# Performance work log

Measured on AMD Instinct MI355X. Metric: run time of the kernel, lower is better.

The kernel has to match this reference:

```python
import jax, jax.numpy as jnp
import numpy as np

N = 100000   # total nodes in batch
E = 1200000  # total edges
D = 64       # dim_features (== hidden_dim)
H = 64       # hidden_dim
T = 32       # dim_targets
L = 3        # num_layers
G = 500      # number of graphs in batch


def setup_inputs() -> dict:
    key = jax.random.key(0)
    ks = jax.random.split(key, 16)
    s = 0.1
    inp = {
        "x": jax.random.normal(ks[0], (N, D), jnp.float32),
        "src": jax.random.randint(ks[1], (E,), 0, N, jnp.int32),
        "dst": jax.random.randint(ks[2], (E,), 0, N, jnp.int32),
        "graph_ids": jnp.sort(jax.random.randint(ks[3], (N,), 0, G, jnp.int32)),
        # GINConv learnable eps (init 0)
        "eps": jnp.zeros((L,), jnp.float32),
        # per-layer conv apply MLP: Linear(D->H), ReLU, Linear(H->H)
        "conv_w1": jax.random.normal(ks[4], (L, D, H), jnp.float32) * s,
        "conv_b1": jnp.zeros((L, H), jnp.float32),
        "conv_w2": jax.random.normal(ks[5], (L, H, H), jnp.float32) * s,
        "conv_b2": jnp.zeros((L, H), jnp.float32),
        # GraphNorm params
        "gn_weight": jnp.ones((L, H), jnp.float32),
        "gn_bias": jnp.zeros((L, H), jnp.float32),
        "gn_scale": jnp.ones((L, H), jnp.float32),
        # per-layer projection MLP: Linear(H->H), ReLU, Linear(H->T)
        "proj_w1": jax.random.normal(ks[6], (L, H, H), jnp.float32) * s,
        "proj_b1": jnp.zeros((L, H), jnp.float32),
        "proj_w2": jax.random.normal(ks[7], (L, H, T), jnp.float32) * s,
        "proj_b2": jnp.zeros((L, T), jnp.float32),
    }
    return inp


def reference(x, src, dst, graph_ids, eps, conv_w1, conv_b1, conv_w2, conv_b2,
              gn_weight, gn_bias, gn_scale, proj_w1, proj_b1, proj_w2, proj_b2):
    gid = graph_ids
    counts = jax.ops.segment_sum(jnp.ones((N,), x.dtype), gid, num_segments=G)
    safe = jnp.maximum(counts, 1.0)[:, None]  # [G,1] nodes per graph

    feat = x
    outs = []
    for l in range(L):
        # GINConv: (1+eps)*h_i + sum over incoming neighbors
        agg = jax.ops.segment_sum(feat[src], dst, num_segments=N)
        h = (1.0 + eps[l]) * feat + agg
        h = jnp.maximum(h @ conv_w1[l] + conv_b1[l], 0.0) @ conv_w2[l] + conv_b2[l]
        # GraphNorm: per-graph mean/std
        mean = jax.ops.segment_sum(h, gid, num_segments=G) / safe
        sub = h - mean[gid] * gn_scale[l]
        var = jax.ops.segment_sum(sub * sub, gid, num_segments=G) / safe
        std = jnp.sqrt(var + 1e-8)
        h = gn_weight[l] * sub / std[gid] + gn_bias[l]
        feat = jnp.maximum(h, 0.0)
        # projection MLP + per-graph mean pooling
        z = jnp.maximum(feat @ proj_w1[l] + proj_b1[l], 0.0) @ proj_w2[l] + proj_b2[l]
        outs.append(jax.ops.segment_sum(z, gid, num_segments=G) / safe)
    return jnp.concatenate(outs, axis=-1)  # [G, L*T]
```

## Files before the change

kernel.cpp:

```cpp
#include <hip/hip_runtime.h>
#include <math.h>

#define N_NODES 100000
#define N_EDGES 1200000
#define DIM 64
#define TDIM 32
#define NLAYERS 3
#define NGRAPH 500
#define NP (N_NODES + 1)

#define BUCKW 512
#define NBUCK ((N_NODES + BUCKW - 1) / BUCKW)
#define ECHUNK ((N_EDGES + 255) / 256)

typedef unsigned short bfu;
typedef __attribute__((ext_vector_type(8))) short short8;
typedef __attribute__((ext_vector_type(4))) float v4f;

__device__ __forceinline__ float bf2f(bfu u) {
    union { unsigned int i; float f; } v; v.i = ((unsigned int)u) << 16; return v.f;
}
__device__ __forceinline__ float bflo(unsigned int d) {
    union { unsigned int i; float f; } v; v.i = d << 16; return v.f;
}
__device__ __forceinline__ float bfhi(unsigned int d) {
    union { unsigned int i; float f; } v; v.i = d & 0xFFFF0000u; return v.f;
}
__device__ __forceinline__ bfu f2bf(float f) {
    union { float f; unsigned int i; } v; v.f = f;
    unsigned int r = v.i + 0x7FFFu + ((v.i >> 16) & 1u);
    return (bfu)(r >> 16);
}


__global__ __launch_bounds__(512) void k_graph_start(const int* __restrict__ gid,
                                                     int* __restrict__ gstart,
                                                     float* __restrict__ inv_safe) {
    int t = threadIdx.x;
    if (t <= NGRAPH) {
        int lo = 0, hi = N_NODES;
        while (lo < hi) {
            int mid = (lo + hi) >> 1;
            if (gid[mid] < t) lo = mid + 1; else hi = mid;
        }
        gstart[t] = lo;
    }
    __syncthreads();
    if (t < NGRAPH) {
        int c = gstart[t + 1] - gstart[t];
        inv_safe[t] = 1.0f / (float)(c > 1 ? c : 1);
    }
}

__global__ __launch_bounds__(256) void k_wprep(const float* __restrict__ w1, const float* __restrict__ w2,
                                               const float* __restrict__ q1, const float* __restrict__ q2,
                                               bfu* __restrict__ w1t, bfu* __restrict__ w2t,
                                               bfu* __restrict__ q1t, bfu* __restrict__ q2t) {
    int i = blockIdx.x * 256 + threadIdx.x;
    if (i < NLAYERS * 4096) {
        int l = i >> 12, k = (i >> 6) & 63, n = i & 63;
        int o = (l << 12) | (n << 6) | k;
        w1t[o] = f2bf(w1[i]);
        w2t[o] = f2bf(w2[i]);
        q1t[o] = f2bf(q1[i]);
    }
    if (i < NLAYERS * 2048) {
        int l = i >> 11, rem = i & 2047, k = rem >> 5, n = rem & 31;
        q2t[l * 2048 + n * 64 + k] = f2bf(q2[i]);
    }
}


__global__ __launch_bounds__(256) void k_bhist(const int* __restrict__ dst, int* __restrict__ bcnt) {
    __shared__ int h[NBUCK];
    int t = threadIdx.x;
    for (int i = t; i < NBUCK; i += 256) h[i] = 0;
    __syncthreads();
    int e0 = blockIdx.x * ECHUNK;
    int e1 = e0 + ECHUNK; if (e1 > N_EDGES) e1 = N_EDGES;
    for (int e = e0 + t; e < e1; e += 256) atomicAdd(&h[dst[e] >> 9], 1);
    __syncthreads();
    for (int i = t; i < NBUCK; i += 256) if (h[i]) atomicAdd(&bcnt[i], h[i]);
}

__global__ __launch_bounds__(256) void k_bscan(const int* __restrict__ bcnt,
                                               int* __restrict__ bbase, int* __restrict__ bcursor) {
    __shared__ int s[256];
    int t = threadIdx.x;
    s[t] = (t < NBUCK) ? bcnt[t] : 0;
    __syncthreads();
    for (int off = 1; off < 256; off <<= 1) {
        int v = (t >= off) ? s[t - off] : 0;
        __syncthreads();
        s[t] += v;
        __syncthreads();
    }
    int ex = t ? s[t - 1] : 0;
    if (t < NBUCK) { bbase[t] = ex; bcursor[t] = ex; }
    if (t == 0) bbase[NBUCK] = N_EDGES;
}

__global__ __launch_bounds__(256) void k_bscatter(const int* __restrict__ src, const int* __restrict__ dst,
                                                  int* __restrict__ bcursor, int2* __restrict__ ebuf) {
    __shared__ int cnt[NBUCK];
    __shared__ int base[NBUCK];
    int t = threadIdx.x;
    for (int i = t; i < NBUCK; i += 256) cnt[i] = 0;
    __syncthreads();
    int e0 = blockIdx.x * ECHUNK;
    int e1 = e0 + ECHUNK; if (e1 > N_EDGES) e1 = N_EDGES;
    for (int e = e0 + t; e < e1; e += 256) atomicAdd(&cnt[dst[e] >> 9], 1);
    __syncthreads();
    for (int i = t; i < NBUCK; i += 256) base[i] = cnt[i] ? atomicAdd(&bcursor[i], cnt[i]) : 0;
    __syncthreads();
    for (int i = t; i < NBUCK; i += 256) cnt[i] = 0;
    __syncthreads();
    for (int e = e0 + t; e < e1; e += 256) {
        int d = dst[e];
        int b = d >> 9;
        int r = atomicAdd(&cnt[b], 1);
        ebuf[base[b] + r] = make_int2(src[e], d);
    }
}

__global__ __launch_bounds__(256) void k_bcsr(const int2* __restrict__ ebuf, const int* __restrict__ bbase,
                                              int* __restrict__ offs, int* __restrict__ csr) {
    __shared__ int ldeg[BUCKW];
    __shared__ int lscan[BUCKW];
    __shared__ int lcur[BUCKW];
    int t = threadIdx.x;
    int b = blockIdx.x;
    int nbase = b << 9;
    int ebeg = bbase[b], eend = bbase[b + 1];
    ldeg[t] = 0; ldeg[t + 256] = 0;
    __syncthreads();
    for (int e = ebeg + t; e < eend; e += 256) atomicAdd(&ldeg[ebuf[e].y - nbase], 1);
    __syncthreads();
    lscan[t] = ldeg[t]; lscan[t + 256] = ldeg[t + 256];
    __syncthreads();
    for (int off = 1; off < BUCKW; off <<= 1) {
        int i0 = t, i1 = t + 256;
        int v0 = (i0 >= off) ? lscan[i0 - off] : 0;
        int v1 = (i1 >= off) ? lscan[i1 - off] : 0;
        __syncthreads();
        lscan[i0] += v0; lscan[i1] += v1;
        __syncthreads();
    }
    int ex0 = lscan[t] - ldeg[t];
    int ex1 = lscan[t + 256] - ldeg[t + 256];
    lcur[t] = ex0; lcur[t + 256] = ex1;
    int n0 = nbase + t, n1 = nbase + t + 256;
    if (n0 < N_NODES) offs[n0] = ebeg + ex0;
    if (n1 < N_NODES) offs[n1] = ebeg + ex1;
    if (b == 0 && t == 0) offs[N_NODES] = N_EDGES;
    __syncthreads();
    for (int e = ebeg + t; e < eend; e += 256) {
        int2 p = ebuf[e];
        int slot = atomicAdd(&lcur[p.y - nbase], 1);
        csr[ebeg + slot] = p.x;
    }
}

__global__ __launch_bounds__(256) void k_x2bf(const float* __restrict__ x, bfu* __restrict__ xb) {
    int i = blockIdx.x * 256 + threadIdx.x;
    int base = i * 4;
    float4 v = *(const float4*)&x[base];
    ushort4 o;
    o.x = f2bf(v.x); o.y = f2bf(v.y); o.z = f2bf(v.z); o.w = f2bf(v.w);
    *(ushort4*)&xb[base] = o;
}

__device__ __forceinline__ void accum8(float* acc, uint4 d) {
    acc[0] += bflo(d.x); acc[1] += bfhi(d.x);
    acc[2] += bflo(d.y); acc[3] += bfhi(d.y);
    acc[4] += bflo(d.z); acc[5] += bfhi(d.z);
    acc[6] += bflo(d.w); acc[7] += bfhi(d.w);
}

__global__ __launch_bounds__(256) void k_agg(const bfu* __restrict__ feat, const int* __restrict__ offs,
                                             const int* __restrict__ csr, const float* __restrict__ eps,
                                             int l, bfu* __restrict__ hin) {
    int w = threadIdx.x >> 6;
    int lane = threadIdx.x & 63;
    int node = blockIdx.x * 4 + w;
    if (node >= N_NODES) return;
    int eidx = lane >> 3;
    int chunk = lane & 7;
    int coff = chunk * 8;
    int e0 = offs[node], e1 = offs[node + 1];
    int eL = e1 - 1;
    float acc[8] = {0.f, 0.f, 0.f, 0.f, 0.f, 0.f, 0.f, 0.f};

    for (int e = e0; e < e1; e += 16) {
        int ea = e + eidx;
        int ca = (ea < eL) ? ea : eL;
        int sa = csr[ca];
        uint4 da = *(const uint4*)&feat[sa * DIM + coff];
        bool two = (e + 8) < e1;
        if (two) {
            int ebi = e + 8 + eidx;
            int cb = (ebi < eL) ? ebi : eL;
            int sb = csr[cb];
            uint4 db = *(const uint4*)&feat[sb * DIM + coff];
            if (ea >= e1) da = make_uint4(0u, 0u, 0u, 0u);
            if (ebi >= e1) db = make_uint4(0u, 0u, 0u, 0u);
            accum8(acc, da);
            accum8(acc, db);
        } else {
            if (ea >= e1) da = make_uint4(0u, 0u, 0u, 0u);
            accum8(acc, da);
        }
    }

#pragma unroll
    for (int j = 0; j < 8; j++) {
        float v = acc[j];
        v += __shfl_xor(v, 8, 64);
        v += __shfl_xor(v, 16, 64);
        v += __shfl_xor(v, 32, 64);
        acc[j] = v;
    }

    float ep = 1.0f + eps[l];
    uint4 s = *(const uint4*)&feat[node * DIM + coff];
    float r0 = ep * bflo(s.x) + acc[0], r1 = ep * bfhi(s.x) + acc[1];
    float r2 = ep * bflo(s.y) + acc[2], r3 = ep * bfhi(s.y) + acc[3];
    float r4 = ep * bflo(s.z) + acc[4], r5 = ep * bfhi(s.z) + acc[5];
    float r6 = ep * bflo(s.w) + acc[6], r7 = ep * bfhi(s.w) + acc[7];
    if (eidx == 0) {
        uint4 o;
        o.x = ((unsigned int)f2bf(r1) << 16) | f2bf(r0);
        o.y = ((unsigned int)f2bf(r3) << 16) | f2bf(r2);
        o.z = ((unsigned int)f2bf(r5) << 16) | f2bf(r4);
        o.w = ((unsigned int)f2bf(r7) << 16) | f2bf(r6);
        *(uint4*)&hin[node * DIM + coff] = o;
    }
}

__global__ __launch_bounds__(256) void k_mlp(const bfu* __restrict__ hin,
                                             const bfu* __restrict__ w1t, const float* __restrict__ b1,
                                             const bfu* __restrict__ w2t, const float* __restrict__ b2,
                                             bfu* __restrict__ hout) {
    __shared__ bfu ldsT[4][16 * 80];
    int t = threadIdx.x;
    int w = t >> 6, lane = t & 63, m = lane & 15, q = lane >> 4;
    int row0 = blockIdx.x * 64;
    int row = row0 + w * 16 + m;
    bool valid = row < N_NODES;

    short8 a0 = {0, 0, 0, 0, 0, 0, 0, 0}, a1 = a0;
    if (valid) {
        a0 = *(const short8*)&hin[row * 64 + q * 8];
        a1 = *(const short8*)&hin[row * 64 + 32 + q * 8];
    }
    short8 bf1[4][2], bf2[4][2];
#pragma unroll
    for (int ct = 0; ct < 4; ct++)
#pragma unroll
        for (int kk = 0; kk < 2; kk++) {
            bf1[ct][kk] = *(const short8*)&w1t[(ct * 16 + m) * 64 + kk * 32 + q * 8];
            bf2[ct][kk] = *(const short8*)&w2t[(ct * 16 + m) * 64 + kk * 32 + q * 8];
        }

    bfu* tl = ldsT[w];
#pragma unroll
    for (int ct = 0; ct < 4; ct++) {
        float bv = b1[ct * 16 + m];
        v4f acc = {bv, bv, bv, bv};
        acc = __builtin_amdgcn_mfma_f32_16x16x32_bf16(a0, bf1[ct][0], acc, 0, 0, 0);
        acc = __builtin_amdgcn_mfma_f32_16x16x32_bf16(a1, bf1[ct][1], acc, 0, 0, 0);
#pragma unroll
        for (int r = 0; r < 4; r++)
            tl[(q * 4 + r) * 80 + ct * 16 + m] = f2bf(fmaxf(acc[r], 0.f));
    }
    short8 a20 = *(short8*)&tl[m * 80 + q * 8];
    short8 a21 = *(short8*)&tl[m * 80 + 32 + q * 8];
#pragma unroll
    for (int ct = 0; ct < 4; ct++) {
        float bv = b2[ct * 16 + m];
        v4f acc = {bv, bv, bv, bv};
        acc = __builtin_amdgcn_mfma_f32_16x16x32_bf16(a20, bf2[ct][0], acc, 0, 0, 0);
        acc = __builtin_amdgcn_mfma_f32_16x16x32_bf16(a21, bf2[ct][1], acc, 0, 0, 0);
#pragma unroll
        for (int r = 0; r < 4; r++)
            tl[(q * 4 + r) * 80 + ct * 16 + m] = f2bf(acc[r]);
    }
#pragma unroll
    for (int i = 0; i < 2; i++) {
        int idx = i * 64 + lane;
        int r = idx >> 3, ch = (idx & 7) * 8;
        int grow = row0 + w * 16 + r;
        uint4 v = *(uint4*)&tl[r * 80 + ch];
        if (grow < N_NODES) *(uint4*)&hout[grow * 64 + ch] = v;
    }
}

__global__ __launch_bounds__(256) void k_stats(const bfu* __restrict__ h,
                                               const int* __restrict__ gstart,
                                               const float* __restrict__ inv_safe,
                                               const float* __restrict__ gnw, const float* __restrict__ gns,
                                               const float* __restrict__ pb2,
                                               float* __restrict__ gms, float* __restrict__ gcoef,
                                               float* __restrict__ out, int l) {
    __shared__ float sRS[4][64];
    __shared__ float sRQ[4][64];
    int t = threadIdx.x;
    int g = blockIdx.x;
    int s = gstart[g], e = gstart[g + 1];
    int nn = e - s;
    float inv = inv_safe[g];
    int lane = t & 63, q = t >> 6;
    float sum = 0.f, sumsq = 0.f;
    for (int i = s + q; i < e; i += 4) {
        float v = bf2f(h[i * 64 + lane]);
        sum += v;
        sumsq += v * v;
    }
    sRS[q][lane] = sum;
    sRQ[q][lane] = sumsq;
    __syncthreads();
    if (t < 64) {
        float S = sRS[0][t] + sRS[1][t] + sRS[2][t] + sRS[3][t];
        float Q = sRQ[0][t] + sRQ[1][t] + sRQ[2][t] + sRQ[3][t];
        float m = S * inv;
        float ms = m * gns[t];
        float var = (Q - 2.f * ms * S + (float)nn * ms * ms) * inv;
        gms[g * 64 + t] = ms;
        gcoef[g * 64 + t] = gnw[t] * rsqrtf(var + 1e-8f);
    }
    if (t < TDIM) {
        out[g * (NLAYERS * TDIM) + l * TDIM + t] = (nn > 0) ? pb2[t] : 0.f;
    }
}

__global__ __launch_bounds__(256) void k_apply_proj(const bfu* __restrict__ h,
                                                    const int* __restrict__ gid,
                                                    const float* __restrict__ gms,
                                                    const float* __restrict__ gcoef,
                                                    const float* __restrict__ gnb,
                                                    const float* __restrict__ inv_safe,
                                                    const bfu* __restrict__ p1t, const float* __restrict__ pb1,
                                                    const bfu* __restrict__ p2t,
                                                    bfu* __restrict__ feat, float* __restrict__ out, int l) {
    __shared__ bfu ldsT[4][16 * 80];
    __shared__ float sZ[64 * 33];
    __shared__ int sGid[64];
    int t = threadIdx.x;
    int w = t >> 6, lane = t & 63, m = lane & 15, q = lane >> 4;
    int row0 = blockIdx.x * 64;
    int row = row0 + w * 16 + m;
    bool valid = row < N_NODES;
    if (t < 64) sGid[t] = (row0 + t < N_NODES) ? gid[row0 + t] : -1;

    union Pack { short8 v; bfu u[8]; uint4 qv; };
    Pack a0, a1;
    a0.qv = make_uint4(0u, 0u, 0u, 0u);
    a1.qv = make_uint4(0u, 0u, 0u, 0u);
    if (valid) {
        int g = gid[row];
#pragma unroll
        for (int kk = 0; kk < 2; kk++) {
            int ch = kk * 32 + q * 8;
            uint4 hv = *(const uint4*)&h[row * 64 + ch];
            float4 msa = *(const float4*)&gms[g * 64 + ch];
            float4 msb = *(const float4*)&gms[g * 64 + ch + 4];
            float4 cfa = *(const float4*)&gcoef[g * 64 + ch];
            float4 cfb = *(const float4*)&gcoef[g * 64 + ch + 4];
            float4 gba = *(const float4*)&gnb[ch];
            float4 gbb = *(const float4*)&gnb[ch + 4];
            Pack& a = kk ? a1 : a0;
            a.u[0] = f2bf(fmaxf(cfa.x * (bflo(hv.x) - msa.x) + gba.x, 0.f));
            a.u[1] = f2bf(fmaxf(cfa.y * (bfhi(hv.x) - msa.y) + gba.y, 0.f));
            a.u[2] = f2bf(fmaxf(cfa.z * (bflo(hv.y) - msa.z) + gba.z, 0.f));
            a.u[3] = f2bf(fmaxf(cfa.w * (bfhi(hv.y) - msa.w) + gba.w, 0.f));
            a.u[4] = f2bf(fmaxf(cfb.x * (bflo(hv.z) - msb.x) + gbb.x, 0.f));
            a.u[5] = f2bf(fmaxf(cfb.y * (bfhi(hv.z) - msb.y) + gbb.y, 0.f));
            a.u[6] = f2bf(fmaxf(cfb.z * (bflo(hv.w) - msb.z) + gbb.z, 0.f));
            a.u[7] = f2bf(fmaxf(cfb.w * (bfhi(hv.w) - msb.w) + gbb.w, 0.f));
            *(uint4*)&feat[row * 64 + ch] = a.qv;
        }
    }

    short8 bf1[4][2], bf2[2][2];
#pragma unroll
    for (int ct = 0; ct < 4; ct++)
#pragma unroll
        for (int kk = 0; kk < 2; kk++)
            bf1[ct][kk] = *(const short8*)&p1t[(ct * 16 + m) * 64 + kk * 32 + q * 8];
#pragma unroll
    for (int ct = 0; ct < 2; ct++)
#pragma unroll
        for (int kk = 0; kk < 2; kk++)
            bf2[ct][kk] = *(const short8*)&p2t[(ct * 16 + m) * 64 + kk * 32 + q * 8];

    bfu* tl = ldsT[w];
#pragma unroll
    for (int ct = 0; ct < 4; ct++) {
        float bv = pb1[ct * 16 + m];
        v4f acc = {bv, bv, bv, bv};
        acc = __builtin_amdgcn_mfma_f32_16x16x32_bf16(a0.v, bf1[ct][0], acc, 0, 0, 0);
        acc = __builtin_amdgcn_mfma_f32_16x16x32_bf16(a1.v, bf1[ct][1], acc, 0, 0, 0);
#pragma unroll
        for (int r = 0; r < 4; r++)
            tl[(q * 4 + r) * 80 + ct * 16 + m] = f2bf(fmaxf(acc[r], 0.f));
    }
    short8 a20 = *(short8*)&tl[m * 80 + q * 8];
    short8 a21 = *(short8*)&tl[m * 80 + 32 + q * 8];
#pragma unroll
    for (int ct = 0; ct < 2; ct++) {
        v4f acc = {0.f, 0.f, 0.f, 0.f};
        acc = __builtin_amdgcn_mfma_f32_16x16x32_bf16(a20, bf2[ct][0], acc, 0, 0, 0);
        acc = __builtin_amdgcn_mfma_f32_16x16x32_bf16(a21, bf2[ct][1], acc, 0, 0, 0);
#pragma unroll
        for (int r = 0; r < 4; r++)
            sZ[(w * 16 + q * 4 + r) * 33 + ct * 16 + m] = acc[r];
    }
    __syncthreads();

    if (t < 32) {
        int cur = sGid[0];
        float a = 0.f;
        for (int r = 0; r < 64; r++) {
            int g2 = sGid[r];
            if (g2 != cur) {
                if (cur >= 0) atomicAdd(&out[cur * (NLAYERS * TDIM) + l * TDIM + t], a * inv_safe[cur]);
                cur = g2;
                a = 0.f;
            }
            if (g2 >= 0) a += sZ[r * 33 + t];
        }
        if (cur >= 0) atomicAdd(&out[cur * (NLAYERS * TDIM) + l * TDIM + t], a * inv_safe[cur]);
    }
}


extern "C" void kernel_launch(void* const* d_in, const int* in_sizes, int n_in,
                              void* d_out, int out_size, void* d_ws, size_t ws_size,
                              hipStream_t stream) {
    const float* x        = (const float*)d_in[0];
    const int*   src      = (const int*)d_in[1];
    const int*   dst      = (const int*)d_in[2];
    const int*   gid      = (const int*)d_in[3];
    const float* eps      = (const float*)d_in[4];
    const float* conv_w1  = (const float*)d_in[5];
    const float* conv_b1  = (const float*)d_in[6];
    const float* conv_w2  = (const float*)d_in[7];
    const float* conv_b2  = (const float*)d_in[8];
    const float* gn_w     = (const float*)d_in[9];
    const float* gn_b     = (const float*)d_in[10];
    const float* gn_s     = (const float*)d_in[11];
    const float* proj_w1  = (const float*)d_in[12];
    const float* proj_b1  = (const float*)d_in[13];
    const float* proj_w2  = (const float*)d_in[14];
    const float* proj_b2  = (const float*)d_in[15];
    float* out = (float*)d_out;

    char* ws = (char*)d_ws;
    size_t off = 0;
    auto alloc = [&](size_t bytes) { char* p = ws + off; off += (bytes + 255) & ~(size_t)255; return p; };
    int*   offs     = (int*)alloc(NP * sizeof(int));
    int*   gstart   = (int*)alloc((NGRAPH + 1) * sizeof(int));
    float* inv_safe = (float*)alloc(NGRAPH * sizeof(float));
    int*   bcnt     = (int*)alloc(NBUCK * sizeof(int));
    int*   bbase    = (int*)alloc((NBUCK + 1) * sizeof(int));
    int*   bcursor  = (int*)alloc(NBUCK * sizeof(int));
    int*   csr      = (int*)alloc(N_EDGES * sizeof(int));
    bfu*   featbf   = (bfu*)alloc((size_t)N_NODES * DIM * sizeof(bfu));
    bfu*   hinbf    = (bfu*)alloc((size_t)N_NODES * DIM * sizeof(bfu));
    bfu*   hbufbf   = (bfu*)alloc((size_t)N_NODES * DIM * sizeof(bfu));
    float* gms      = (float*)alloc((size_t)NGRAPH * 64 * sizeof(float));
    float* gcoef    = (float*)alloc((size_t)NGRAPH * 64 * sizeof(float));
    bfu*   w1t      = (bfu*)alloc((size_t)NLAYERS * 4096 * sizeof(bfu));
    bfu*   w2t      = (bfu*)alloc((size_t)NLAYERS * 4096 * sizeof(bfu));
    bfu*   p1t      = (bfu*)alloc((size_t)NLAYERS * 4096 * sizeof(bfu));
    bfu*   p2t      = (bfu*)alloc((size_t)NLAYERS * 2048 * sizeof(bfu));
    int2*  ebuf     = (int2*)alloc((size_t)N_EDGES * sizeof(int2));

    k_graph_start<<<1, 512, 0, stream>>>(gid, gstart, inv_safe);
    hipMemsetAsync(bcnt, 0, NBUCK * sizeof(int), stream);
    k_bhist<<<256, 256, 0, stream>>>(dst, bcnt);
    k_bscan<<<1, 256, 0, stream>>>(bcnt, bbase, bcursor);
    k_bscatter<<<256, 256, 0, stream>>>(src, dst, bcursor, ebuf);
    k_bcsr<<<NBUCK, 256, 0, stream>>>(ebuf, bbase, offs, csr);
    k_x2bf<<<(N_NODES * DIM / 4) / 256, 256, 0, stream>>>(x, featbf);
    k_wprep<<<48, 256, 0, stream>>>(conv_w1, conv_w2, proj_w1, proj_w2, w1t, w2t, p1t, p2t);

    int aggbl = (N_NODES + 3) / 4;
    int mlpbl = (N_NODES + 63) / 64;
    for (int l = 0; l < NLAYERS; l++) {
        k_agg<<<aggbl, 256, 0, stream>>>(featbf, offs, csr, eps, l, hinbf);
        k_mlp<<<mlpbl, 256, 0, stream>>>(hinbf, w1t + l * 4096, conv_b1 + l * 64,
                                         w2t + l * 4096, conv_b2 + l * 64, hbufbf);
        k_stats<<<NGRAPH, 256, 0, stream>>>(hbufbf, gstart, inv_safe,
                                            gn_w + l * 64, gn_s + l * 64, proj_b2 + l * 32,
                                            gms, gcoef, out, l);
        k_apply_proj<<<mlpbl, 256, 0, stream>>>(hbufbf, gid, gms, gcoef, gn_b + l * 64,
                                                inv_safe, p1t + l * 4096, proj_b1 + l * 64,
                                                p2t + l * 2048, featbf, out, l);
    }
}
```

Before: 455.3 us.

## Fuse aggregation, conv MLP and GraphNorm stats; merge setup kernels

Neighbour aggregation is merged into the conv MLP kernel. Each wave aggregates its 16 nodes into LDS and then runs the MFMA MLP, so the hin round-trip through global memory goes away. Per-graph sum and sum-of-squares are now accumulated with atomics in the MLP epilogue instead of a separate pass that re-reads h, and a small finalize kernel computes the coefficients and zeros the accumulators. The setup kernels (x to bf16, graph starts, weight prep) are combined into one launch. The cost is less parallelism during aggregation, since each wave now handles 16 nodes one after another, plus float atomic contention.

Result: slower. 474.8 us (+4.3%).

```diff
diff --git a/kernel.cpp b/kernel.cpp
--- a/kernel.cpp
+++ b/kernel.cpp
@@ -12,6 +12,7 @@
 #define BUCKW 512
 #define NBUCK ((N_NODES + BUCKW - 1) / BUCKW)
 #define ECHUNK ((N_EDGES + 255) / 256)
+#define MLPBL ((N_NODES + 63) / 64)
 
 typedef unsigned short bfu;
 typedef __attribute__((ext_vector_type(8))) short short8;
@@ -32,41 +33,45 @@
     return (bfu)(r >> 16);
 }
 
-
-__global__ __launch_bounds__(512) void k_graph_start(const int* __restrict__ gid,
-                                                     int* __restrict__ gstart,
-                                                     float* __restrict__ inv_safe) {
-    int t = threadIdx.x;
-    if (t <= NGRAPH) {
-        int lo = 0, hi = N_NODES;
-        while (lo < hi) {
-            int mid = (lo + hi) >> 1;
-            if (gid[mid] < t) lo = mid + 1; else hi = mid;
-        }
-        gstart[t] = lo;
-    }
-    __syncthreads();
-    if (t < NGRAPH) {
-        int c = gstart[t + 1] - gstart[t];
-        inv_safe[t] = 1.0f / (float)(c > 1 ? c : 1);
-    }
-}
-
-__global__ __launch_bounds__(256) void k_wprep(const float* __restrict__ w1, const float* __restrict__ w2,
+__global__ __launch_bounds__(256) void k_setup(const float* __restrict__ x, bfu* __restrict__ xb,
+                                               const int* __restrict__ gid, int* __restrict__ gstart,
+                                               float* __restrict__ inv_safe,
+                                               const float* __restrict__ w1, const float* __restrict__ w2,
                                                const float* __restrict__ q1, const float* __restrict__ q2,
                                                bfu* __restrict__ w1t, bfu* __restrict__ w2t,
                                                bfu* __restrict__ q1t, bfu* __restrict__ q2t) {
-    int i = blockIdx.x * 256 + threadIdx.x;
-    if (i < NLAYERS * 4096) {
+    int b = blockIdx.x, t = threadIdx.x;
+    if (b < 6250) {
+        int base = (b * 256 + t) * 4;
+        float4 v = *(const float4*)&x[base];
+        ushort4 o;
+        o.x = f2bf(v.x); o.y = f2bf(v.y); o.z = f2bf(v.z); o.w = f2bf(v.w);
+        *(ushort4*)&xb[base] = o;
+    } else if (b == 6250) {
+        for (int tt = t; tt <= NGRAPH; tt += 256) {
+            int lo = 0, hi = N_NODES;
+            while (lo < hi) {
+                int mid = (lo + hi) >> 1;
+                if (gid[mid] < tt) lo = mid + 1; else hi = mid;
+            }
+            gstart[tt] = lo;
+        }
+        __syncthreads();
+        for (int tt = t; tt < NGRAPH; tt += 256) {
+            int c = gstart[tt + 1] - gstart[tt];
+            inv_safe[tt] = 1.0f / (float)(c > 1 ? c : 1);
+        }
+    } else {
+        int i = (b - 6251) * 256 + t;
         int l = i >> 12, k = (i >> 6) & 63, n = i & 63;
         int o = (l << 12) | (n << 6) | k;
         w1t[o] = f2bf(w1[i]);
         w2t[o] = f2bf(w2[i]);
         q1t[o] = f2bf(q1[i]);
-    }
-    if (i < NLAYERS * 2048) {
-        int l = i >> 11, rem = i & 2047, k = rem >> 5, n = rem & 31;
-        q2t[l * 2048 + n * 64 + k] = f2bf(q2[i]);
+        if (i < NLAYERS * 2048) {
+            int l2 = i >> 11, rem = i & 2047, k2 = rem >> 5, n2 = rem & 31;
+            q2t[l2 * 2048 + n2 * 64 + k2] = f2bf(q2[i]);
+        }
     }
 }
 
@@ -161,15 +166,6 @@
     }
 }
 
-__global__ __launch_bounds__(256) void k_x2bf(const float* __restrict__ x, bfu* __restrict__ xb) {
-    int i = blockIdx.x * 256 + threadIdx.x;
-    int base = i * 4;
-    float4 v = *(const float4*)&x[base];
-    ushort4 o;
-    o.x = f2bf(v.x); o.y = f2bf(v.y); o.z = f2bf(v.z); o.w = f2bf(v.w);
-    *(ushort4*)&xb[base] = o;
-}
-
 __device__ __forceinline__ void accum8(float* acc, uint4 d) {
     acc[0] += bflo(d.x); acc[1] += bfhi(d.x);
     acc[2] += bflo(d.y); acc[3] += bfhi(d.y);
@@ -177,82 +173,74 @@
     acc[6] += bflo(d.w); acc[7] += bfhi(d.w);
 }
 
-__global__ __launch_bounds__(256) void k_agg(const bfu* __restrict__ feat, const int* __restrict__ offs,
-                                             const int* __restrict__ csr, const float* __restrict__ eps,
-                                             int l, bfu* __restrict__ hin) {
-    int w = threadIdx.x >> 6;
-    int lane = threadIdx.x & 63;
-    int node = blockIdx.x * 4 + w;
-    if (node >= N_NODES) return;
-    int eidx = lane >> 3;
-    int chunk = lane & 7;
-    int coff = chunk * 8;
-    int e0 = offs[node], e1 = offs[node + 1];
-    int eL = e1 - 1;
-    float acc[8] = {0.f, 0.f, 0.f, 0.f, 0.f, 0.f, 0.f, 0.f};
-
-    for (int e = e0; e < e1; e += 16) {
-        int ea = e + eidx;
-        int ca = (ea < eL) ? ea : eL;
-        int sa = csr[ca];
-        uint4 da = *(const uint4*)&feat[sa * DIM + coff];
-        bool two = (e + 8) < e1;
-        if (two) {
-            int ebi = e + 8 + eidx;
-            int cb = (ebi < eL) ? ebi : eL;
-            int sb = csr[cb];
-            uint4 db = *(const uint4*)&feat[sb * DIM + coff];
-            if (ea >= e1) da = make_uint4(0u, 0u, 0u, 0u);
-            if (ebi >= e1) db = make_uint4(0u, 0u, 0u, 0u);
-            accum8(acc, da);
-            accum8(acc, db);
-        } else {
-            if (ea >= e1) da = make_uint4(0u, 0u, 0u, 0u);
-            accum8(acc, da);
-        }
-    }
-
-#pragma unroll
-    for (int j = 0; j < 8; j++) {
-        float v = acc[j];
-        v += __shfl_xor(v, 8, 64);
-        v += __shfl_xor(v, 16, 64);
-        v += __shfl_xor(v, 32, 64);
-        acc[j] = v;
-    }
-
+__global__ __launch_bounds__(256, 4) void k_agg_mlp(const bfu* __restrict__ feat,
+                                                    const int* __restrict__ offs, const int* __restrict__ csr,
+                                                    const float* __restrict__ eps, int l,
+                                                    const bfu* __restrict__ w1t, const float* __restrict__ b1,
+                                                    const bfu* __restrict__ w2t, const float* __restrict__ b2,
+                                                    const int* __restrict__ gid,
+                                                    bfu* __restrict__ hout,
+                                                    float* __restrict__ gsum, float* __restrict__ gsq) {
+    __shared__ bfu ldsT[4][16 * 80];
+    __shared__ int sG[4][16];
+    int t = threadIdx.x;
+    int w = t >> 6, lane = t & 63, m = lane & 15, q = lane >> 4;
+    int nbase = blockIdx.x * 64 + w * 16;
+    bfu* my = ldsT[w];
+    int eidx = lane >> 3, chunk = lane & 7, coff = chunk * 8;
     float ep = 1.0f + eps[l];
-    uint4 s = *(const uint4*)&feat[node * DIM + coff];
-    float r0 = ep * bflo(s.x) + acc[0], r1 = ep * bfhi(s.x) + acc[1];
-    float r2 = ep * bflo(s.y) + acc[2], r3 = ep * bfhi(s.y) + acc[3];
-    float r4 = ep * bflo(s.z) + acc[4], r5 = ep * bfhi(s.z) + acc[5];
-    float r6 = ep * bflo(s.w) + acc[6], r7 = ep * bfhi(s.w) + acc[7];
-    if (eidx == 0) {
-        uint4 o;
-        o.x = ((unsigned int)f2bf(r1) << 16) | f2bf(r0);
-        o.y = ((unsigned int)f2bf(r3) << 16) | f2bf(r2);
-        o.z = ((unsigned int)f2bf(r5) << 16) | f2bf(r4);
-        o.w = ((unsigned int)f2bf(r7) << 16) | f2bf(r6);
-        *(uint4*)&hin[node * DIM + coff] = o;
-    }
-}
-
-__global__ __launch_bounds__(256) void k_mlp(const bfu* __restrict__ hin,
-                                             const bfu* __restrict__ w1t, const float* __restrict__ b1,
-                                             const bfu* __restrict__ w2t, const float* __restrict__ b2,
-                                             bfu* __restrict__ hout) {
-    __shared__ bfu ldsT[4][16 * 80];
-    int t = threadIdx.x;
-    int w = t >> 6, lane = t & 63, m = lane & 15, q = lane >> 4;
-    int row0 = blockIdx.x * 64;
-    int row = row0 + w * 16 + m;
-    bool valid = row < N_NODES;
-
-    short8 a0 = {0, 0, 0, 0, 0, 0, 0, 0}, a1 = a0;
-    if (valid) {
-        a0 = *(const short8*)&hin[row * 64 + q * 8];
-        a1 = *(const short8*)&hin[row * 64 + 32 + q * 8];
-    }
+
+    if (lane < 16) sG[w][lane] = (nbase + lane < N_NODES) ? gid[nbase + lane] : -1;
+
+    for (int i = 0; i < 16; i++) {
+        int node = nbase + i;
+        if (node >= N_NODES) break;
+        int e0 = offs[node], e1 = offs[node + 1];
+        int eL = e1 - 1;
+        float acc[8] = {0.f, 0.f, 0.f, 0.f, 0.f, 0.f, 0.f, 0.f};
+        for (int e = e0; e < e1; e += 16) {
+            int ea = e + eidx;
+            int ca = (ea < eL) ? ea : eL;
+            int sa = csr[ca];
+            uint4 da = *(const uint4*)&feat[sa * DIM + coff];
+            bool two = (e + 8) < e1;
+            if (two) {
+                int ebi = e + 8 + eidx;
+                int cb = (ebi < eL) ? ebi : eL;
+                int sb = csr[cb];
+                uint4 db = *(const uint4*)&feat[sb * DIM + coff];
+                if (ea >= e1) da = make_uint4(0u, 0u, 0u, 0u);
+                if (ebi >= e1) db = make_uint4(0u, 0u, 0u, 0u);
+                accum8(acc, da);
+                accum8(acc, db);
+            } else {
+                if (ea >= e1) da = make_uint4(0u, 0u, 0u, 0u);
+                accum8(acc, da);
+            }
+        }
+#pragma unroll
+        for (int j = 0; j < 8; j++) {
+            float v = acc[j];
+            v += __shfl_xor(v, 8, 64);
+            v += __shfl_xor(v, 16, 64);
+            v += __shfl_xor(v, 32, 64);
+            acc[j] = v;
+        }
+        uint4 s = *(const uint4*)&feat[node * DIM + coff];
+        float r0 = ep * bflo(s.x) + acc[0], r1 = ep * bfhi(s.x) + acc[1];
+        float r2 = ep * bflo(s.y) + acc[2], r3 = ep * bfhi(s.y) + acc[3];
+        float r4 = ep * bflo(s.z) + acc[4], r5 = ep * bfhi(s.z) + acc[5];
+        float r6 = ep * bflo(s.w) + acc[6], r7 = ep * bfhi(s.w) + acc[7];
+        if (eidx == 0) {
+            uint4 o;
+            o.x = ((unsigned int)f2bf(r1) << 16) | f2bf(r0);
+            o.y = ((unsigned int)f2bf(r3) << 16) | f2bf(r2);
+            o.z = ((unsigned int)f2bf(r5) << 16) | f2bf(r4);
+            o.w = ((unsigned int)f2bf(r7) << 16) | f2bf(r6);
+            *(uint4*)&my[i * 80 + coff] = o;
+        }
+    }
+
     short8 bf1[4][2], bf2[4][2];
 #pragma unroll
     for (int ct = 0; ct < 4; ct++)
@@ -262,7 +250,8 @@
             bf2[ct][kk] = *(const short8*)&w2t[(ct * 16 + m) * 64 + kk * 32 + q * 8];
         }
 
-    bfu* tl = ldsT[w];
+    short8 a0 = *(short8*)&my[m * 80 + q * 8];
+    short8 a1 = *(short8*)&my[m * 80 + 32 + q * 8];
 #pragma unroll
     for (int ct = 0; ct < 4; ct++) {
         float bv = b1[ct * 16 + m];
@@ -271,10 +260,10 @@
         acc = __builtin_amdgcn_mfma_f32_16x16x32_bf16(a1, bf1[ct][1], acc, 0, 0, 0);
 #pragma unroll
         for (int r = 0; r < 4; r++)
-            tl[(q * 4 + r) * 80 + ct * 16 + m] = f2bf(fmaxf(acc[r], 0.f));
-    }
-    short8 a20 = *(short8*)&tl[m * 80 + q * 8];
-    short8 a21 = *(short8*)&tl[m * 80 + 32 + q * 8];
+            my[(q * 4 + r) * 80 + ct * 16 + m] = f2bf(fmaxf(acc[r], 0.f));
+    }
+    short8 a20 = *(short8*)&my[m * 80 + q * 8];
+    short8 a21 = *(short8*)&my[m * 80 + 32 + q * 8];
 #pragma unroll
     for (int ct = 0; ct < 4; ct++) {
         float bv = b2[ct * 16 + m];
@@ -283,54 +272,59 @@
         acc = __builtin_amdgcn_mfma_f32_16x16x32_bf16(a21, bf2[ct][1], acc, 0, 0, 0);
 #pragma unroll
         for (int r = 0; r < 4; r++)
-            tl[(q * 4 + r) * 80 + ct * 16 + m] = f2bf(acc[r]);
+            my[(q * 4 + r) * 80 + ct * 16 + m] = f2bf(acc[r]);
     }
 #pragma unroll
     for (int i = 0; i < 2; i++) {
         int idx = i * 64 + lane;
         int r = idx >> 3, ch = (idx & 7) * 8;
-        int grow = row0 + w * 16 + r;
-        uint4 v = *(uint4*)&tl[r * 80 + ch];
+        int grow = nbase + r;
+        uint4 v = *(uint4*)&my[r * 80 + ch];
         if (grow < N_NODES) *(uint4*)&hout[grow * 64 + ch] = v;
     }
-}
-
-__global__ __launch_bounds__(256) void k_stats(const bfu* __restrict__ h,
-                                               const int* __restrict__ gstart,
-                                               const float* __restrict__ inv_safe,
-                                               const float* __restrict__ gnw, const float* __restrict__ gns,
-                                               const float* __restrict__ pb2,
-                                               float* __restrict__ gms, float* __restrict__ gcoef,
-                                               float* __restrict__ out, int l) {
-    __shared__ float sRS[4][64];
-    __shared__ float sRQ[4][64];
-    int t = threadIdx.x;
-    int g = blockIdx.x;
-    int s = gstart[g], e = gstart[g + 1];
-    int nn = e - s;
+    float s_acc = 0.f, q_acc = 0.f;
+    int cur = sG[w][0];
+    for (int r = 0; r < 16; r++) {
+        int g2 = sG[w][r];
+        if (g2 != cur) {
+            if (cur >= 0) {
+                atomicAdd(&gsum[cur * 64 + lane], s_acc);
+                atomicAdd(&gsq[cur * 64 + lane], q_acc);
+            }
+            cur = g2; s_acc = 0.f; q_acc = 0.f;
+        }
+        if (g2 >= 0) {
+            float v = bf2f(my[r * 80 + lane]);
+            s_acc += v; q_acc += v * v;
+        }
+    }
+    if (cur >= 0) {
+        atomicAdd(&gsum[cur * 64 + lane], s_acc);
+        atomicAdd(&gsq[cur * 64 + lane], q_acc);
+    }
+}
+
+__global__ __launch_bounds__(256) void k_stats_fin(const int* __restrict__ gstart,
+                                                   const float* __restrict__ inv_safe,
+                                                   const float* __restrict__ gnw, const float* __restrict__ gns,
+                                                   const float* __restrict__ pb2,
+                                                   float* __restrict__ gsum, float* __restrict__ gsq,
+                                                   float* __restrict__ gms, float* __restrict__ gcoef,
+                                                   float* __restrict__ out, int l) {
+    int t = threadIdx.x;
+    int g = blockIdx.x * 4 + (t >> 6);
+    int c = t & 63;
+    int nn = gstart[g + 1] - gstart[g];
     float inv = inv_safe[g];
-    int lane = t & 63, q = t >> 6;
-    float sum = 0.f, sumsq = 0.f;
-    for (int i = s + q; i < e; i += 4) {
-        float v = bf2f(h[i * 64 + lane]);
-        sum += v;
-        sumsq += v * v;
-    }
-    sRS[q][lane] = sum;
-    sRQ[q][lane] = sumsq;
-    __syncthreads();
-    if (t < 64) {
-        float S = sRS[0][t] + sRS[1][t] + sRS[2][t] + sRS[3][t];
-        float Q = sRQ[0][t] + sRQ[1][t] + sRQ[2][t] + sRQ[3][t];
-        float m = S * inv;
-        float ms = m * gns[t];
-        float var = (Q - 2.f * ms * S + (float)nn * ms * ms) * inv;
-        gms[g * 64 + t] = ms;
-        gcoef[g * 64 + t] = gnw[t] * rsqrtf(var + 1e-8f);
-    }
-    if (t < TDIM) {
-        out[g * (NLAYERS * TDIM) + l * TDIM + t] = (nn > 0) ? pb2[t] : 0.f;
-    }
+    float S = gsum[g * 64 + c], Q = gsq[g * 64 + c];
+    gsum[g * 64 + c] = 0.f;
+    gsq[g * 64 + c] = 0.f;
+    float mean = S * inv;
+    float ms = mean * gns[c];
+    float var = (Q - 2.f * ms * S + (float)nn * ms * ms) * inv;
+    gms[g * 64 + c] = ms;
+    gcoef[g * 64 + c] = gnw[c] * rsqrtf(var + 1e-8f);
+    if (c < TDIM) out[g * (NLAYERS * TDIM) + l * TDIM + c] = (nn > 0) ? pb2[c] : 0.f;
 }
 
 __global__ __launch_bounds__(256) void k_apply_proj(const bfu* __restrict__ h,
@@ -466,8 +460,9 @@
     int*   bcursor  = (int*)alloc(NBUCK * sizeof(int));
     int*   csr      = (int*)alloc(N_EDGES * sizeof(int));
     bfu*   featbf   = (bfu*)alloc((size_t)N_NODES * DIM * sizeof(bfu));
-    bfu*   hinbf    = (bfu*)alloc((size_t)N_NODES * DIM * sizeof(bfu));
     bfu*   hbufbf   = (bfu*)alloc((size_t)N_NODES * DIM * sizeof(bfu));
+    float* gsum     = (float*)alloc((size_t)NGRAPH * 64 * sizeof(float));
+    float* gsq      = (float*)alloc((size_t)NGRAPH * 64 * sizeof(float));
     float* gms      = (float*)alloc((size_t)NGRAPH * 64 * sizeof(float));
     float* gcoef    = (float*)alloc((size_t)NGRAPH * 64 * sizeof(float));
     bfu*   w1t      = (bfu*)alloc((size_t)NLAYERS * 4096 * sizeof(bfu));
@@ -476,25 +471,23 @@
     bfu*   p2t      = (bfu*)alloc((size_t)NLAYERS * 2048 * sizeof(bfu));
     int2*  ebuf     = (int2*)alloc((size_t)N_EDGES * sizeof(int2));
 
-    k_graph_start<<<1, 512, 0, stream>>>(gid, gstart, inv_safe);
     hipMemsetAsync(bcnt, 0, NBUCK * sizeof(int), stream);
+    hipMemsetAsync(gsum, 0, 2 * NGRAPH * 64 * sizeof(float), stream);
+    k_setup<<<6299, 256, 0, stream>>>(x, featbf, gid, gstart, inv_safe,
+                                      conv_w1, conv_w2, proj_w1, proj_w2, w1t, w2t, p1t, p2t);
     k_bhist<<<256, 256, 0, stream>>>(dst, bcnt);
     k_bscan<<<1, 256, 0, stream>>>(bcnt, bbase, bcursor);
     k_bscatter<<<256, 256, 0, stream>>>(src, dst, bcursor, ebuf);
     k_bcsr<<<NBUCK, 256, 0, stream>>>(ebuf, bbase, offs, csr);
-    k_x2bf<<<(N_NODES * DIM / 4) / 256, 256, 0, stream>>>(x, featbf);
-    k_wprep<<<48, 256, 0, stream>>>(conv_w1, conv_w2, proj_w1, proj_w2, w1t, w2t, p1t, p2t);
-
-    int aggbl = (N_NODES + 3) / 4;
-    int mlpbl = (N_NODES + 63) / 64;
+
     for (int l = 0; l < NLAYERS; l++) {
-        k_agg<<<aggbl, 256, 0, stream>>>(featbf, offs, csr, eps, l, hinbf);
-        k_mlp<<<mlpbl, 256, 0, stream>>>(hinbf, w1t + l * 4096, conv_b1 + l * 64,
-                                         w2t + l * 4096, conv_b2 + l * 64, hbufbf);
-        k_stats<<<NGRAPH, 256, 0, stream>>>(hbufbf, gstart, inv_safe,
-                                            gn_w + l * 64, gn_s + l * 64, proj_b2 + l * 32,
-                                            gms, gcoef, out, l);
-        k_apply_proj<<<mlpbl, 256, 0, stream>>>(hbufbf, gid, gms, gcoef, gn_b + l * 64,
+        k_agg_mlp<<<MLPBL, 256, 0, stream>>>(featbf, offs, csr, eps, l,
+                                             w1t + l * 4096, conv_b1 + l * 64,
+                                             w2t + l * 4096, conv_b2 + l * 64,
+                                             gid, hbufbf, gsum, gsq);
+        k_stats_fin<<<125, 256, 0, stream>>>(gstart, inv_safe, gn_w + l * 64, gn_s + l * 64,
+                                             proj_b2 + l * 32, gsum, gsq, gms, gcoef, out, l);
+        k_apply_proj<<<MLPBL, 256, 0, stream>>>(hbufbf, gid, gms, gcoef, gn_b + l * 64,
                                                 inv_safe, p1t + l * 4096, proj_b1 + l * 64,
                                                 p2t + l * 2048, featbf, out, l);
     }
```
